# Kernel tuning notes

Hardware: AMD Instinct MI355X
Metric: run time of the kernel (lower is better)

The kernel has to match this reference:

```python
import jax, jax.numpy as jnp
import numpy as np

N_NODES = 50000
N_EDGES = 800000
NODE_DIM = 128
EDGE_IN = 31
EMB_DIM = 128
GATE_HID = 128
INIT_GATE_BIAS = 2.0


def setup_inputs() -> dict:
    key = jax.random.key(0)
    ks = jax.random.split(key, 8)
    x = jax.random.normal(ks[0], (N_NODES, NODE_DIM), dtype=jnp.float32)
    edge_attr = jax.random.normal(ks[1], (N_EDGES, EDGE_IN), dtype=jnp.float32)
    edge_index = jax.random.randint(ks[2], (2, N_EDGES), 0, N_NODES, dtype=jnp.int64)
    gate_in_dim = 2 * NODE_DIM + EDGE_IN
    # params (torch.nn.Linear-style scaled uniform init)
    def lin(k, fan_in, fan_out):
        bound = 1.0 / np.sqrt(fan_in)
        kw, kb = jax.random.split(k)
        W = jax.random.uniform(kw, (fan_in, fan_out), minval=-bound, maxval=bound, dtype=jnp.float32)
        b = jax.random.uniform(kb, (fan_out,), minval=-bound, maxval=bound, dtype=jnp.float32)
        return W, b
    W_proj, b_proj = lin(ks[3], EDGE_IN, EMB_DIM)
    W1, b1 = lin(ks[4], gate_in_dim, GATE_HID)
    W2, _ = lin(ks[5], GATE_HID, 1)
    b2 = jnp.full((1,), INIT_GATE_BIAS, dtype=jnp.float32)
    return {
        "x": x,
        "edge_attr": edge_attr,
        "edge_index": edge_index,
        "W_proj": W_proj,
        "b_proj": b_proj,
        "W1": W1,
        "b1": b1,
        "W2": W2,
        "b2": b2,
    }


def reference(x, edge_attr, edge_index, W_proj, b_proj, W1, b1, W2, b2):
    src = edge_index[0]
    dst = edge_index[1]
    xu = x[src]                      # [E, node_dim] gather
    xv = x[dst]                      # [E, node_dim] gather
    base = edge_attr @ W_proj + b_proj            # [E, emb_dim]
    gate_in = jnp.concatenate([xu, xv, edge_attr], axis=-1)  # [E, 2*node_dim+31]
    h = jax.nn.gelu(gate_in @ W1 + b1)            # [E, gate_hidden]
    gate = jax.nn.sigmoid(h @ W2 + b2)            # [E, 1]
    return base * gate                            # [E, emb_dim]
```

## Files before the change

kernel.cpp:

```cpp
#include <hip/hip_runtime.h>
#include <math.h>

#define N_NODES 50000
#define N_EDGES 800000

typedef __attribute__((ext_vector_type(8))) short bf16x8;
typedef __attribute__((ext_vector_type(4))) float f32x4;

__device__ __forceinline__ unsigned f2bfu(float f) {
  union { float f; unsigned u; } v; v.f = f;
  return (v.u + 0x7FFFu + ((v.u >> 16) & 1u)) >> 16;
}
__device__ __forceinline__ short f2bf(float f) { return (short)f2bfu(f); }

__device__ __forceinline__ float bflo(unsigned d) {
  union { unsigned u; float f; } v; v.u = d << 16; return v.f;
}
__device__ __forceinline__ float bfhi(unsigned d) {
  union { unsigned u; float f; } v; v.u = d & 0xFFFF0000u; return v.f;
}

__device__ __forceinline__ float gelu_f(float h) {
  const float m1 = h * h;
  const float t2u = h * fmaf(0.07135481f, m1, 1.5957691f);
  const float e = __expf(t2u);
  const float rc = __builtin_amdgcn_rcpf(1.f + e);
  return h - h * rc;
}

#define PIN(v) asm volatile("" : "+v"(v))

__global__ __launch_bounds__(256) void node_kernel(
    const float* __restrict__ x, const float* __restrict__ W1,
    const float* __restrict__ b1, unsigned short* __restrict__ AB) {
  const int l = threadIdx.x & 63;
  const int wv = threadIdx.x >> 6;
  const int r = l & 15, g4 = l >> 4;

  const int wid = blockIdx.x * 4 + wv;
  const int s = wid & 3;

  bf16x8 wA[4][4];
#pragma unroll
  for (int q = 0; q < 4; ++q) {
    const int c = 16 * (4 * s + q) + r;
    const float* Wb = (c < 128) ? (W1 + c) : (W1 + 128 * 128 + (c - 128));
#pragma unroll
    for (int ks = 0; ks < 4; ++ks) {
#pragma unroll
      for (int t = 0; t < 8; ++t)
        wA[q][ks][t] = f2bf(Wb[(size_t)(ks * 32 + g4 * 8 + t) * 128]);
      PIN(wA[q][ks]);
    }
  }
  float4 bv[4];
#pragma unroll
  for (int q = 0; q < 4; ++q)
    bv[q] = *(const float4*)(b1 + ((16 * (4 * s + q) + g4 * 4) & 127));

  const int half = s >> 1;

  for (int t0 = wid >> 2; t0 < (N_NODES / 16); t0 += 1024) {
    const int n0 = t0 * 16;
    f32x4 acc[4] = {{0,0,0,0},{0,0,0,0},{0,0,0,0},{0,0,0,0}};
#pragma unroll
    for (int ks = 0; ks < 4; ++ks) {
      const float* xr = x + (size_t)(n0 + r) * 128 + ks * 32 + g4 * 8;
      const float4 x0 = *(const float4*)xr;
      const float4 x1 = *(const float4*)(xr + 4);
      bf16x8 xb;
      xb[0] = f2bf(x0.x); xb[1] = f2bf(x0.y); xb[2] = f2bf(x0.z); xb[3] = f2bf(x0.w);
      xb[4] = f2bf(x1.x); xb[5] = f2bf(x1.y); xb[6] = f2bf(x1.z); xb[7] = f2bf(x1.w);
#pragma unroll
      for (int q = 0; q < 4; ++q)
        acc[q] = __builtin_amdgcn_mfma_f32_16x16x32_bf16(wA[q][ks], xb, acc[q], 0, 0, 0);
    }
#pragma unroll
    for (int q = 0; q < 4; ++q) {
      const int mb8 = 4 * (s & 1) + q;
      const float o0 = acc[q][0] + 0.5f * bv[q].x;
      const float o1 = acc[q][1] + 0.5f * bv[q].y;
      const float o2 = acc[q][2] + 0.5f * bv[q].z;
      const float o3 = acc[q][3] + 0.5f * bv[q].w;
      uint2 pk;
      pk.x = f2bfu(o0) | (f2bfu(o1) << 16);
      pk.y = f2bfu(o2) | (f2bfu(o3) << 16);
      *(uint2*)(AB + (size_t)(n0 + r) * 256 + half * 128 + g4 * 32 + mb8 * 4) = pk;
    }
  }
}

#define ROWD 132

__global__ __launch_bounds__(256) void edge_kernel(
    const float* __restrict__ edge_attr, const int* __restrict__ edge_index,
    const unsigned short* __restrict__ AB,
    const float* __restrict__ W_proj, const float* __restrict__ b_proj,
    const float* __restrict__ W1,
    const float* __restrict__ W2, const float* __restrict__ b2,
    float* __restrict__ out) {
  __shared__ float tlds[4][16 * ROWD];
  const int l = threadIdx.x & 63;
  const int wv = threadIdx.x >> 6;
  const int r = l & 15, g4 = l >> 4;
  float* const tl = &tlds[wv][0];

  bf16x8 wP[8], wH[8];
#pragma unroll
  for (int mb = 0; mb < 8; ++mb) {
    const int c = 16 * mb + r;
    bf16x8 p, h;
#pragma unroll
    for (int t = 0; t < 8; ++t) {
      const int kk = g4 * 8 + t;
      p[t] = (kk < 31) ? f2bf(W_proj[(size_t)kk * 128 + c]) : (short)0;
      h[t] = (kk < 31) ? f2bf(W1[(size_t)(256 + kk) * 128 + c]) : (short)0;
    }
    wP[mb] = p; wH[mb] = h;
    PIN(wP[mb]); PIN(wH[mb]);
  }
  const float b2v = b2[0];

  const int nwaves = gridDim.x * 4;
  const int NT = N_EDGES / 16;

  for (int tile = blockIdx.x * 4 + wv; tile < NT; tile += nwaves) {
    const int e = tile * 16 + r;
    const int src = edge_index[e];
    const int dst = edge_index[N_EDGES + e];

    const float* ear = edge_attr + (size_t)e * 31 + g4 * 8;
    bf16x8 eb;
#pragma unroll
    for (int t = 0; t < 8; ++t) {
      const int kk = g4 * 8 + t;
      eb[t] = (kk < 31) ? f2bf(ear[t]) : (short)0;
    }

    const uint4* ap4 = (const uint4*)(AB + (size_t)src * 256 + g4 * 32);
    const uint4* bp4 = (const uint4*)(AB + (size_t)dst * 256 + 128 + g4 * 32);
    uint4 ua[4], ub[4];
#pragma unroll
    for (int t = 0; t < 4; ++t) { ua[t] = ap4[t]; ub[t] = bp4[t]; }

    f32x4 acch[8];
#pragma unroll
    for (int t = 0; t < 4; ++t) {
      acch[2 * t][0]     = bflo(ua[t].x) + bflo(ub[t].x);
      acch[2 * t][1]     = bfhi(ua[t].x) + bfhi(ub[t].x);
      acch[2 * t][2]     = bflo(ua[t].y) + bflo(ub[t].y);
      acch[2 * t][3]     = bfhi(ua[t].y) + bfhi(ub[t].y);
      acch[2 * t + 1][0] = bflo(ua[t].z) + bflo(ub[t].z);
      acch[2 * t + 1][1] = bfhi(ua[t].z) + bfhi(ub[t].z);
      acch[2 * t + 1][2] = bflo(ua[t].w) + bflo(ub[t].w);
      acch[2 * t + 1][3] = bfhi(ua[t].w) + bfhi(ub[t].w);
    }
#pragma unroll
    for (int mb = 0; mb < 8; ++mb)
      acch[mb] = __builtin_amdgcn_mfma_f32_16x16x32_bf16(wH[mb], eb, acch[mb], 0, 0, 0);

    float lg = 0.f;
#pragma unroll
    for (int mb = 0; mb < 8; ++mb) {
      const float4 w2v = *(const float4*)(W2 + 16 * mb + g4 * 4);
      lg = fmaf(gelu_f(acch[mb][0]), w2v.x, lg);
      lg = fmaf(gelu_f(acch[mb][1]), w2v.y, lg);
      lg = fmaf(gelu_f(acch[mb][2]), w2v.z, lg);
      lg = fmaf(gelu_f(acch[mb][3]), w2v.w, lg);
    }
    lg += __shfl_xor(lg, 16);
    lg += __shfl_xor(lg, 32);
    const float gate = __builtin_amdgcn_rcpf(1.f + __expf(-(lg + b2v)));

#pragma unroll
    for (int mb = 0; mb < 8; ++mb) {
      f32x4 ac = __builtin_amdgcn_mfma_f32_16x16x32_bf16(
          wP[mb], eb, (f32x4){0.f, 0.f, 0.f, 0.f}, 0, 0, 0);
      const float4 bp = *(const float4*)(b_proj + 16 * mb + g4 * 4);
      f32x4 o;
      o[0] = (ac[0] + bp.x) * gate;
      o[1] = (ac[1] + bp.y) * gate;
      o[2] = (ac[2] + bp.z) * gate;
      o[3] = (ac[3] + bp.w) * gate;
      *(f32x4*)(tl + ROWD * r + 16 * mb + 4 * g4) = o;
    }

    float* const obase = out + (size_t)tile * 16 * 128;
#pragma unroll
    for (int k = 0; k < 8; ++k) {
      const f32x4 v = *(const f32x4*)(tl + ROWD * (2 * k + (l >> 5)) + 4 * (l & 31));
      __builtin_nontemporal_store(v, (f32x4*)(obase + 256 * k + 4 * l));
    }
  }
}

extern "C" void kernel_launch(void* const* d_in, const int* in_sizes, int n_in,
                              void* d_out, int out_size, void* d_ws, size_t ws_size,
                              hipStream_t stream) {
  const float* x          = (const float*)d_in[0];
  const float* edge_attr  = (const float*)d_in[1];
  const int*   edge_index = (const int*)d_in[2];
  const float* W_proj     = (const float*)d_in[3];
  const float* b_proj     = (const float*)d_in[4];
  const float* W1         = (const float*)d_in[5];
  const float* b1         = (const float*)d_in[6];
  const float* W2         = (const float*)d_in[7];
  const float* b2         = (const float*)d_in[8];
  float* out = (float*)d_out;
  unsigned short* AB = (unsigned short*)d_ws;

  hipLaunchKernelGGL(node_kernel, dim3(1024), dim3(256), 0, stream,
                     x, W1, b1, AB);
  hipLaunchKernelGGL(edge_kernel, dim3(2048), dim3(256), 0, stream,
                     edge_attr, edge_index, AB, W_proj, b_proj, W1, W2, b2,
                     out);
}
```

Before: 172.1 us.

## Transpose edge MFMA orientation, move weights to LDS, store output directly

Swaps the MFMA operand order in the edge kernel so each lane owns output columns across four edges. The node kernel's AB layout is changed to match, so each lane gathers one 16-byte chunk from four different src/dst rows. The weight fragments for the hidden and projection matmuls now live in shared memory instead of registers, which lowers register pressure. The LDS transpose staging for the output is removed in favour of direct scalar stores, which may cost write coalescing, and the gate reduction now takes four shuffle steps per edge.

```diff
diff --git a/kernel.cpp b/kernel.cpp
--- a/kernel.cpp
+++ b/kernel.cpp
@@ -39,6 +39,8 @@
 
   const int wid = blockIdx.x * 4 + wv;
   const int s = wid & 3;
+  const int half = s >> 1;
+  const int sh = s & 1;
 
   bf16x8 wA[4][4];
 #pragma unroll
@@ -53,12 +55,12 @@
       PIN(wA[q][ks]);
     }
   }
-  float4 bv[4];
+  float bva[4][4];
 #pragma unroll
   for (int q = 0; q < 4; ++q)
-    bv[q] = *(const float4*)(b1 + ((16 * (4 * s + q) + g4 * 4) & 127));
-
-  const int half = s >> 1;
+#pragma unroll
+    for (int i = 0; i < 4; ++i)
+      bva[q][i] = 0.5f * b1[(16 * (4 * s + q) + 4 * g4 + i) & 127];
 
   for (int t0 = wid >> 2; t0 < (N_NODES / 16); t0 += 1024) {
     const int n0 = t0 * 16;
@@ -76,21 +78,14 @@
         acc[q] = __builtin_amdgcn_mfma_f32_16x16x32_bf16(wA[q][ks], xb, acc[q], 0, 0, 0);
     }
 #pragma unroll
-    for (int q = 0; q < 4; ++q) {
-      const int mb8 = 4 * (s & 1) + q;
-      const float o0 = acc[q][0] + 0.5f * bv[q].x;
-      const float o1 = acc[q][1] + 0.5f * bv[q].y;
-      const float o2 = acc[q][2] + 0.5f * bv[q].z;
-      const float o3 = acc[q][3] + 0.5f * bv[q].w;
+    for (int i = 0; i < 4; ++i) {
       uint2 pk;
-      pk.x = f2bfu(o0) | (f2bfu(o1) << 16);
-      pk.y = f2bfu(o2) | (f2bfu(o3) << 16);
-      *(uint2*)(AB + (size_t)(n0 + r) * 256 + half * 128 + g4 * 32 + mb8 * 4) = pk;
-    }
-  }
-}
-
-#define ROWD 132
+      pk.x = f2bfu(acc[0][i] + bva[0][i]) | (f2bfu(acc[1][i] + bva[1][i]) << 16);
+      pk.y = f2bfu(acc[2][i] + bva[2][i]) | (f2bfu(acc[3][i] + bva[3][i]) << 16);
+      *(uint2*)(AB + (size_t)(n0 + r) * 256 + half * 128 + (4 * g4 + i) * 8 + 4 * sh) = pk;
+    }
+  }
+}
 
 __global__ __launch_bounds__(256) void edge_kernel(
     const float* __restrict__ edge_attr, const int* __restrict__ edge_index,
@@ -99,37 +94,46 @@
     const float* __restrict__ W1,
     const float* __restrict__ W2, const float* __restrict__ b2,
     float* __restrict__ out) {
-  __shared__ float tlds[4][16 * ROWD];
+  __shared__ uint4 wHl[512];
+  __shared__ uint4 wPl[512];
   const int l = threadIdx.x & 63;
   const int wv = threadIdx.x >> 6;
   const int r = l & 15, g4 = l >> 4;
-  float* const tl = &tlds[wv][0];
-
-  bf16x8 wP[8], wH[8];
+
+#pragma unroll
+  for (int pp = 0; pp < 2; ++pp) {
+    const int id = threadIdx.x * 2 + pp;
+    const int mb = id >> 6, ln = id & 63;
+    const int rr = ln & 15, gg = ln >> 4;
+    union { uint4 u; bf16x8 b; } h, p;
+#pragma unroll
+    for (int t = 0; t < 8; ++t) {
+      const int kk = gg * 8 + t;
+      h.b[t] = (kk < 31) ? f2bf(W1[(size_t)(256 + kk) * 128 + 16 * mb + rr]) : (short)0;
+      p.b[t] = (kk < 31) ? f2bf(W_proj[(size_t)kk * 128 + 16 * mb + rr]) : (short)0;
+    }
+    wHl[id] = h.u;
+    wPl[id] = p.u;
+  }
+
+  float w2r[8], bpr[8];
 #pragma unroll
   for (int mb = 0; mb < 8; ++mb) {
-    const int c = 16 * mb + r;
-    bf16x8 p, h;
-#pragma unroll
-    for (int t = 0; t < 8; ++t) {
-      const int kk = g4 * 8 + t;
-      p[t] = (kk < 31) ? f2bf(W_proj[(size_t)kk * 128 + c]) : (short)0;
-      h[t] = (kk < 31) ? f2bf(W1[(size_t)(256 + kk) * 128 + c]) : (short)0;
-    }
-    wP[mb] = p; wH[mb] = h;
-    PIN(wP[mb]); PIN(wH[mb]);
+    w2r[mb] = W2[16 * mb + r];
+    bpr[mb] = b_proj[16 * mb + r];
   }
   const float b2v = b2[0];
+  __syncthreads();
 
   const int nwaves = gridDim.x * 4;
   const int NT = N_EDGES / 16;
 
   for (int tile = blockIdx.x * 4 + wv; tile < NT; tile += nwaves) {
-    const int e = tile * 16 + r;
-    const int src = edge_index[e];
-    const int dst = edge_index[N_EDGES + e];
-
-    const float* ear = edge_attr + (size_t)e * 31 + g4 * 8;
+    const int e0 = tile * 16 + 4 * g4;
+    const int4 s4 = *(const int4*)(edge_index + e0);
+    const int4 d4 = *(const int4*)(edge_index + N_EDGES + e0);
+
+    const float* ear = edge_attr + (size_t)(tile * 16 + r) * 31 + g4 * 8;
     bf16x8 eb;
 #pragma unroll
     for (int t = 0; t < 8; ++t) {
@@ -137,59 +141,61 @@
       eb[t] = (kk < 31) ? f2bf(ear[t]) : (short)0;
     }
 
-    const uint4* ap4 = (const uint4*)(AB + (size_t)src * 256 + g4 * 32);
-    const uint4* bp4 = (const uint4*)(AB + (size_t)dst * 256 + 128 + g4 * 32);
     uint4 ua[4], ub[4];
-#pragma unroll
-    for (int t = 0; t < 4; ++t) { ua[t] = ap4[t]; ub[t] = bp4[t]; }
+    ua[0] = *(const uint4*)(AB + (size_t)s4.x * 256 + r * 8);
+    ua[1] = *(const uint4*)(AB + (size_t)s4.y * 256 + r * 8);
+    ua[2] = *(const uint4*)(AB + (size_t)s4.z * 256 + r * 8);
+    ua[3] = *(const uint4*)(AB + (size_t)s4.w * 256 + r * 8);
+    ub[0] = *(const uint4*)(AB + (size_t)d4.x * 256 + 128 + r * 8);
+    ub[1] = *(const uint4*)(AB + (size_t)d4.y * 256 + 128 + r * 8);
+    ub[2] = *(const uint4*)(AB + (size_t)d4.z * 256 + 128 + r * 8);
+    ub[3] = *(const uint4*)(AB + (size_t)d4.w * 256 + 128 + r * 8);
 
     f32x4 acch[8];
 #pragma unroll
-    for (int t = 0; t < 4; ++t) {
-      acch[2 * t][0]     = bflo(ua[t].x) + bflo(ub[t].x);
-      acch[2 * t][1]     = bfhi(ua[t].x) + bfhi(ub[t].x);
-      acch[2 * t][2]     = bflo(ua[t].y) + bflo(ub[t].y);
-      acch[2 * t][3]     = bfhi(ua[t].y) + bfhi(ub[t].y);
-      acch[2 * t + 1][0] = bflo(ua[t].z) + bflo(ub[t].z);
-      acch[2 * t + 1][1] = bfhi(ua[t].z) + bfhi(ub[t].z);
-      acch[2 * t + 1][2] = bflo(ua[t].w) + bflo(ub[t].w);
-      acch[2 * t + 1][3] = bfhi(ua[t].w) + bfhi(ub[t].w);
-    }
+    for (int mb = 0; mb < 8; ++mb) {
+      const int dw = mb >> 1;
+#pragma unroll
+      for (int i = 0; i < 4; ++i) {
+        const unsigned da = ((const unsigned*)&ua[i])[dw];
+        const unsigned db = ((const unsigned*)&ub[i])[dw];
+        acch[mb][i] = ((mb & 1) ? bfhi(da) : bflo(da)) +
+                      ((mb & 1) ? bfhi(db) : bflo(db));
+      }
+    }
+
+#pragma unroll
+    for (int mb = 0; mb < 8; ++mb) {
+      union { uint4 u; bf16x8 b; } w;
+      w.u = wHl[mb * 64 + l];
+      acch[mb] = __builtin_amdgcn_mfma_f32_16x16x32_bf16(eb, w.b, acch[mb], 0, 0, 0);
+    }
+
+    float lg[4] = {0.f, 0.f, 0.f, 0.f};
 #pragma unroll
     for (int mb = 0; mb < 8; ++mb)
-      acch[mb] = __builtin_amdgcn_mfma_f32_16x16x32_bf16(wH[mb], eb, acch[mb], 0, 0, 0);
-
-    float lg = 0.f;
+#pragma unroll
+      for (int i = 0; i < 4; ++i)
+        lg[i] = fmaf(gelu_f(acch[mb][i]), w2r[mb], lg[i]);
+#pragma unroll
+    for (int i = 0; i < 4; ++i) {
+      lg[i] += __shfl_xor(lg[i], 1);
+      lg[i] += __shfl_xor(lg[i], 2);
+      lg[i] += __shfl_xor(lg[i], 4);
+      lg[i] += __shfl_xor(lg[i], 8);
+      lg[i] = __builtin_amdgcn_rcpf(1.f + __expf(-(lg[i] + b2v)));
+    }
+
+    float* const obase = out + (size_t)e0 * 128 + r;
 #pragma unroll
     for (int mb = 0; mb < 8; ++mb) {
-      const float4 w2v = *(const float4*)(W2 + 16 * mb + g4 * 4);
-      lg = fmaf(gelu_f(acch[mb][0]), w2v.x, lg);
-      lg = fmaf(gelu_f(acch[mb][1]), w2v.y, lg);
-      lg = fmaf(gelu_f(acch[mb][2]), w2v.z, lg);
-      lg = fmaf(gelu_f(acch[mb][3]), w2v.w, lg);
-    }
-    lg += __shfl_xor(lg, 16);
-    lg += __shfl_xor(lg, 32);
-    const float gate = __builtin_amdgcn_rcpf(1.f + __expf(-(lg + b2v)));
-
-#pragma unroll
-    for (int mb = 0; mb < 8; ++mb) {
+      union { uint4 u; bf16x8 b; } w;
+      w.u = wPl[mb * 64 + l];
       f32x4 ac = __builtin_amdgcn_mfma_f32_16x16x32_bf16(
-          wP[mb], eb, (f32x4){0.f, 0.f, 0.f, 0.f}, 0, 0, 0);
-      const float4 bp = *(const float4*)(b_proj + 16 * mb + g4 * 4);
-      f32x4 o;
-      o[0] = (ac[0] + bp.x) * gate;
-      o[1] = (ac[1] + bp.y) * gate;
-      o[2] = (ac[2] + bp.z) * gate;
-      o[3] = (ac[3] + bp.w) * gate;
-      *(f32x4*)(tl + ROWD * r + 16 * mb + 4 * g4) = o;
-    }
-
-    float* const obase = out + (size_t)tile * 16 * 128;
-#pragma unroll
-    for (int k = 0; k < 8; ++k) {
-      const f32x4 v = *(const f32x4*)(tl + ROWD * (2 * k + (l >> 5)) + 4 * (l & 31));
-      __builtin_nontemporal_store(v, (f32x4*)(obase + 256 * k + 4 * l));
+          eb, w.b, (f32x4){0.f, 0.f, 0.f, 0.f}, 0, 0, 0);
+#pragma unroll
+      for (int i = 0; i < 4; ++i)
+        obase[(size_t)i * 128 + 16 * mb] = (ac[i] + bpr[mb]) * lg[i];
     }
   }
 }
```

After: 222.3 us. +29.2%, slower.

## Precompute edge weight fragments, prefetch edge indices, drop LDS output staging

Applied to the files above, without the earlier changes.

A new single-block kernel converts the edge-side W1 and W_proj slices into bf16 MFMA fragments once, so each edge block loads packed uint4 fragments instead of doing strided fp32 loads and conversions. The edge loop now prefetches src/dst indices for the next tile to hide the index-load latency before the dependent gathers. The LDS transpose and nontemporal coalesced store are replaced by direct per-row float4 stores, which frees shared memory but writes the output in a less coalesced pattern with normal caching.

```diff
diff --git a/kernel.cpp b/kernel.cpp
--- a/kernel.cpp
+++ b/kernel.cpp
@@ -29,6 +29,24 @@
 }
 
 #define PIN(v) asm volatile("" : "+v"(v))
+
+__global__ void wfrag_kernel(const float* __restrict__ W_proj,
+                             const float* __restrict__ W1,
+                             uint4* __restrict__ wfrag) {
+  const int id = threadIdx.x;
+  const int mat = id >> 9;
+  const int fid = id & 511;
+  const int mb = fid >> 6, ln = fid & 63;
+  const int rr = ln & 15, gg = ln >> 4;
+  const float* W = mat ? W_proj : (W1 + (size_t)256 * 128);
+  union { uint4 u; bf16x8 b; } f;
+#pragma unroll
+  for (int t = 0; t < 8; ++t) {
+    const int kk = gg * 8 + t;
+    f.b[t] = (kk < 31) ? f2bf(W[(size_t)kk * 128 + 16 * mb + rr]) : (short)0;
+  }
+  wfrag[id] = f.u;
+}
 
 __global__ __launch_bounds__(256) void node_kernel(
     const float* __restrict__ x, const float* __restrict__ W1,
@@ -90,44 +108,43 @@
   }
 }
 
-#define ROWD 132
-
 __global__ __launch_bounds__(256) void edge_kernel(
     const float* __restrict__ edge_attr, const int* __restrict__ edge_index,
-    const unsigned short* __restrict__ AB,
-    const float* __restrict__ W_proj, const float* __restrict__ b_proj,
-    const float* __restrict__ W1,
-    const float* __restrict__ W2, const float* __restrict__ b2,
-    float* __restrict__ out) {
-  __shared__ float tlds[4][16 * ROWD];
+    const unsigned short* __restrict__ AB, const uint4* __restrict__ wfrag,
+    const float* __restrict__ b_proj, const float* __restrict__ W2,
+    const float* __restrict__ b2, float* __restrict__ out) {
   const int l = threadIdx.x & 63;
   const int wv = threadIdx.x >> 6;
   const int r = l & 15, g4 = l >> 4;
-  float* const tl = &tlds[wv][0];
-
-  bf16x8 wP[8], wH[8];
+
+  bf16x8 wH[8], wP[8];
 #pragma unroll
   for (int mb = 0; mb < 8; ++mb) {
-    const int c = 16 * mb + r;
-    bf16x8 p, h;
-#pragma unroll
-    for (int t = 0; t < 8; ++t) {
-      const int kk = g4 * 8 + t;
-      p[t] = (kk < 31) ? f2bf(W_proj[(size_t)kk * 128 + c]) : (short)0;
-      h[t] = (kk < 31) ? f2bf(W1[(size_t)(256 + kk) * 128 + c]) : (short)0;
-    }
-    wP[mb] = p; wH[mb] = h;
-    PIN(wP[mb]); PIN(wH[mb]);
+    union { uint4 u; bf16x8 b; } h, p;
+    h.u = wfrag[mb * 64 + l];
+    p.u = wfrag[512 + mb * 64 + l];
+    wH[mb] = h.b; wP[mb] = p.b;
+    PIN(wH[mb]); PIN(wP[mb]);
   }
   const float b2v = b2[0];
 
   const int nwaves = gridDim.x * 4;
   const int NT = N_EDGES / 16;
 
-  for (int tile = blockIdx.x * 4 + wv; tile < NT; tile += nwaves) {
+  int tile = blockIdx.x * 4 + wv;
+  if (tile >= NT) return;
+  int src = edge_index[tile * 16 + r];
+  int dst = edge_index[N_EDGES + tile * 16 + r];
+
+  for (; tile < NT; tile += nwaves) {
     const int e = tile * 16 + r;
-    const int src = edge_index[e];
-    const int dst = edge_index[N_EDGES + e];
+    const int cs = src, cd = dst;
+
+    const int tn = tile + nwaves;
+    if (tn < NT) {
+      src = edge_index[tn * 16 + r];
+      dst = edge_index[N_EDGES + tn * 16 + r];
+    }
 
     const float* ear = edge_attr + (size_t)e * 31 + g4 * 8;
     bf16x8 eb;
@@ -137,8 +154,8 @@
       eb[t] = (kk < 31) ? f2bf(ear[t]) : (short)0;
     }
 
-    const uint4* ap4 = (const uint4*)(AB + (size_t)src * 256 + g4 * 32);
-    const uint4* bp4 = (const uint4*)(AB + (size_t)dst * 256 + 128 + g4 * 32);
+    const uint4* ap4 = (const uint4*)(AB + (size_t)cs * 256 + g4 * 32);
+    const uint4* bp4 = (const uint4*)(AB + (size_t)cd * 256 + 128 + g4 * 32);
     uint4 ua[4], ub[4];
 #pragma unroll
     for (int t = 0; t < 4; ++t) { ua[t] = ap4[t]; ub[t] = bp4[t]; }
@@ -172,24 +189,18 @@
     lg += __shfl_xor(lg, 32);
     const float gate = __builtin_amdgcn_rcpf(1.f + __expf(-(lg + b2v)));
 
+    float* const orow = out + (size_t)e * 128 + 4 * g4;
 #pragma unroll
     for (int mb = 0; mb < 8; ++mb) {
       f32x4 ac = __builtin_amdgcn_mfma_f32_16x16x32_bf16(
           wP[mb], eb, (f32x4){0.f, 0.f, 0.f, 0.f}, 0, 0, 0);
-      const float4 bp = *(const float4*)(b_proj + 16 * mb + g4 * 4);
+      const float4 bp = *(const float4*)(b_proj + 16 * mb + 4 * g4);
       f32x4 o;
       o[0] = (ac[0] + bp.x) * gate;
       o[1] = (ac[1] + bp.y) * gate;
       o[2] = (ac[2] + bp.z) * gate;
       o[3] = (ac[3] + bp.w) * gate;
-      *(f32x4*)(tl + ROWD * r + 16 * mb + 4 * g4) = o;
-    }
-
-    float* const obase = out + (size_t)tile * 16 * 128;
-#pragma unroll
-    for (int k = 0; k < 8; ++k) {
-      const f32x4 v = *(const f32x4*)(tl + ROWD * (2 * k + (l >> 5)) + 4 * (l & 31));
-      __builtin_nontemporal_store(v, (f32x4*)(obase + 256 * k + 4 * l));
+      *(f32x4*)(orow + 16 * mb) = o;
     }
   }
 }
@@ -208,10 +219,13 @@
   const float* b2         = (const float*)d_in[8];
   float* out = (float*)d_out;
   unsigned short* AB = (unsigned short*)d_ws;
-
+  uint4* wfrag = (uint4*)(AB + (size_t)N_NODES * 256);
+
+  hipLaunchKernelGGL(wfrag_kernel, dim3(1), dim3(1024), 0, stream,
+                     W_proj, W1, wfrag);
   hipLaunchKernelGGL(node_kernel, dim3(1024), dim3(256), 0, stream,
                      x, W1, b1, AB);
   hipLaunchKernelGGL(edge_kernel, dim3(2048), dim3(256), 0, stream,
-                     edge_attr, edge_index, AB, W_proj, b_proj, W1, W2, b2,
+                     edge_attr, edge_index, AB, wfrag, b_proj, W2, b2,
                      out);
 }
```

Result: slower. 241.2 us (+40.2%).
